# Optimization experiments

Hardware: AMD Instinct MI355X
Metric: run time of the kernel (lower is better)

## Reference

```python
import jax, jax.numpy as jnp
import numpy as np

N, L, S, E, H = 8, 4096, 4096, 256, 8
D = E // H
EPS = 1e-6


def setup_inputs() -> dict:
    key = jax.random.key(0)
    ks = jax.random.split(key, 12)
    sc = 1.0 / np.sqrt(E)
    return {
        "q": jax.random.normal(ks[0], (N, L, E), jnp.float32),
        "k": jax.random.normal(ks[1], (N, S, E), jnp.float32),
        "v": jax.random.normal(ks[2], (N, S, E), jnp.float32),
        "q_mask": jax.random.uniform(ks[3], (N, L)) > 0.2,
        "kv_mask": jax.random.uniform(ks[4], (N, S)) > 0.2,
        "Wq": jax.random.normal(ks[5], (E, E), jnp.float32) * sc,
        "bq": jax.random.normal(ks[6], (E,), jnp.float32) * sc,
        "Wk": jax.random.normal(ks[7], (E, E), jnp.float32) * sc,
        "bk": jax.random.normal(ks[8], (E,), jnp.float32) * sc,
        "Wv": jax.random.normal(ks[9], (E, E), jnp.float32) * sc,
        "bv": jax.random.normal(ks[10], (E,), jnp.float32) * sc,
        "Wm": jax.random.normal(ks[11], (E, E), jnp.float32) * sc,
    }


def reference(q, k, v, q_mask, kv_mask, Wq, bq, Wk, bk, Wv, bv, Wm):
    n, l, _ = q.shape
    s = k.shape[1]
    # QKV projections (torch Linear: x @ W.T + b), split into heads
    Q = (q @ Wq.T + bq).reshape(n, l, H, D)
    K = (k @ Wk.T + bk).reshape(n, s, H, D)
    V = (v @ Wv.T + bv).reshape(n, s, H, D)
    # elu feature map (elu(x) + 1)
    Qf = jax.nn.elu(Q) + 1.0
    Kf = jax.nn.elu(K) + 1.0
    qm = q_mask.astype(Qf.dtype)[:, :, None, None]
    km = kv_mask.astype(Kf.dtype)[:, :, None, None]
    Qf = Qf * qm
    Kf = Kf * km
    Vm = V * km / s  # values / v_length
    # KV aggregation: [n,h,d,v]
    KV = jnp.einsum('nshd,nshv->nhdv', Kf, Vm)
    # normalizer Z: [n,l,h]
    Z = 1.0 / (jnp.einsum('nlhd,nhd->nlh', Qf, Kf.sum(axis=1)) + EPS)
    out = jnp.einsum('nlhd,nhdv->nlhv', Qf, KV) * Z[..., None] * s
    # merge projection (no bias)
    return out.reshape(n, l, H * D) @ Wm.T
```

## Files before the change

### kernel.cpp

```cpp
#include <hip/hip_runtime.h>

#define EPSF 1e-6f

typedef __bf16 bf16;
typedef bf16 bf16x4 __attribute__((ext_vector_type(4)));
typedef bf16 bf16x8 __attribute__((ext_vector_type(8)));
typedef float f32x4 __attribute__((ext_vector_type(4)));


__global__ __launch_bounds__(256) void prep(
    const float* __restrict__ Wq, const float* __restrict__ Wk,
    const float* __restrict__ Wv, const float* __restrict__ Wm,
    bf16* __restrict__ Wb, float4* __restrict__ Z)
{
    const int b = blockIdx.x, t = threadIdx.x;
    if (b < 66) {
        const int i = b * 256 + t;
        if (i < 16896) Z[i] = float4{0.f, 0.f, 0.f, 0.f};
        return;
    }
    const int wi = b - 66;
    const int m  = wi >> 6;
    const float* S = (m == 0) ? Wq : (m == 1) ? Wk : (m == 2) ? Wv : Wm;
    const int idx = (wi & 63) * 1024 + t * 4;
    float4 v = *(const float4*)(S + idx);
    bf16x4 p = {(bf16)v.x, (bf16)v.y, (bf16)v.z, (bf16)v.w};
    *(bf16x4*)(Wb + (size_t)m * 65536 + idx) = p;
}

__global__ __launch_bounds__(256, 2) void kv_fused(
    const float* __restrict__ kin, const float* __restrict__ vin,
    const bf16* __restrict__ Wkb, const bf16* __restrict__ Wvb,
    const float* __restrict__ bk, const float* __restrict__ bv,
    const int* __restrict__ kv_mask,
    float* __restrict__ KV, float* __restrict__ Ksum)
{
    const int n = blockIdx.y, s0 = blockIdx.x * 32;
    const int t = threadIdx.x, lane = t & 63, w = t >> 6;
    const int ln15 = lane & 15, lg = lane >> 4;
    const int wn = w * 64;

    __shared__ bf16 Xs[32][40];
    __shared__ bf16 Ws[256][40];
    __shared__ bf16 KfT[256][40];
    __shared__ bf16 VmT[256][40];

    const int xr = t >> 3, xc = (t & 7) * 4;
    const int wr = t >> 2, wc = (t & 3) * 8;

    for (int g = 0; g < 2; ++g) {
        const float* X  = g ? vin : kin;
        const bf16*  Wg = g ? Wvb : Wkb;
        const float* bg = g ? bv : bk;
        f32x4 acc[2][4] = {};
        for (int k0 = 0; k0 < 256; k0 += 32) {
            float4 xv = *(const float4*)(X + ((size_t)(n * 4096 + s0 + xr)) * 256 + k0 + xc);
            bf16x4 xp = {(bf16)xv.x, (bf16)xv.y, (bf16)xv.z, (bf16)xv.w};
            *(bf16x4*)&Xs[xr][xc] = xp;
            #pragma unroll
            for (int i = 0; i < 4; ++i)
                *(bf16x8*)&Ws[wr + 64 * i][wc] =
                    *(const bf16x8*)(Wg + (size_t)(wr + 64 * i) * 256 + k0 + wc);
            __syncthreads();
            bf16x8 a[2], bfr[4];
            a[0] = *(const bf16x8*)&Xs[ln15][lg * 8];
            a[1] = *(const bf16x8*)&Xs[16 + ln15][lg * 8];
            #pragma unroll
            for (int ni = 0; ni < 4; ++ni)
                bfr[ni] = *(const bf16x8*)&Ws[wn + ni * 16 + ln15][lg * 8];
            #pragma unroll
            for (int mi = 0; mi < 2; ++mi)
                #pragma unroll
                for (int ni = 0; ni < 4; ++ni)
                    acc[mi][ni] = __builtin_amdgcn_mfma_f32_16x16x32_bf16(
                        a[mi], bfr[ni], acc[mi][ni], 0, 0, 0);
            __syncthreads();
        }
        bf16 (*T)[40] = g ? VmT : KfT;
        #pragma unroll
        for (int ni = 0; ni < 4; ++ni) {
            const int col = wn + ni * 16 + ln15;
            const float bias = bg[col];
            float red = 0.f;
            #pragma unroll
            for (int mi = 0; mi < 2; ++mi) {
                const int sb = mi * 16 + lg * 4;
                bf16x4 pk;
                #pragma unroll
                for (int r = 0; r < 4; ++r) {
                    float x = acc[mi][ni][r] + bias;
                    if (g == 0) x = (x > 0.f) ? (x + 1.f) : __expf(x);
                    x *= kv_mask[n * 4096 + s0 + sb + r] ? 1.f : 0.f;
                    red += x;
                    pk[r] = (bf16)x;
                }
                *(bf16x4*)&T[col][sb] = pk;
            }
            if (g == 0) {
                red += __shfl_xor(red, 16);
                red += __shfl_xor(red, 32);
                if (lane < 16) atomicAdd(Ksum + n * 256 + col, red);
            }
        }
        __syncthreads();
    }
    #pragma unroll
    for (int hh = 0; hh < 2; ++hh) {
        const int h = w * 2 + hh;
        bf16x8 a[2], bb[2];
        #pragma unroll
        for (int mi = 0; mi < 2; ++mi)
            a[mi] = *(const bf16x8*)&VmT[h * 32 + mi * 16 + ln15][lg * 8];
        #pragma unroll
        for (int ni = 0; ni < 2; ++ni)
            bb[ni] = *(const bf16x8*)&KfT[h * 32 + ni * 16 + ln15][lg * 8];
        float* base = KV + (size_t)(n * 8 + h) * 1024;
        #pragma unroll
        for (int mi = 0; mi < 2; ++mi)
            #pragma unroll
            for (int ni = 0; ni < 2; ++ni) {
                f32x4 c = {};
                c = __builtin_amdgcn_mfma_f32_16x16x32_bf16(a[mi], bb[ni], c, 0, 0, 0);
                const int d = ni * 16 + ln15;
                #pragma unroll
                for (int r = 0; r < 4; ++r) {
                    const int v = mi * 16 + lg * 4 + r;
                    atomicAdd(base + v * 32 + d, c[r]);
                }
            }
    }
}

__global__ __launch_bounds__(256, 2) void attn_fused(
    const float* __restrict__ qin, const bf16* __restrict__ Wqb,
    const float* __restrict__ bq, const int* __restrict__ q_mask,
    const bf16* __restrict__ Wmb,
    const float* __restrict__ KV, const float* __restrict__ Ksum,
    float* __restrict__ out)
{
    const int n = blockIdx.y, l0 = blockIdx.x * 32;
    const int t = threadIdx.x, lane = t & 63, w = t >> 6;
    const int ln15 = lane & 15, lg = lane >> 4;
    const int wn = w * 64;

    __shared__ bf16  Xs[32][40];
    __shared__ bf16  Ws[256][40];
    __shared__ bf16  Qs[32][264];
    __shared__ bf16  KVs[8][32][40];
    __shared__ float KSs[256];
    __shared__ float Dens[32][8];

    {
        const float* kvn = KV + (size_t)n * 8192;
        #pragma unroll
        for (int i = 0; i < 8; ++i) {
            const int idx = (t * 8 + i) * 4;
            float4 vv = *(const float4*)(kvn + idx);
            bf16x4 p = {(bf16)vv.x, (bf16)vv.y, (bf16)vv.z, (bf16)vv.w};
            const int h = idx >> 10, rem = idx & 1023;
            *(bf16x4*)&KVs[h][rem >> 5][rem & 31] = p;
        }
        KSs[t] = Ksum[n * 256 + t];
    }
    {
        const int xr = t >> 3, xc = (t & 7) * 4, wr = t >> 2, wc = (t & 3) * 8;
        f32x4 acc[2][4] = {};
        for (int k0 = 0; k0 < 256; k0 += 32) {
            float4 xv = *(const float4*)(qin + ((size_t)(n * 4096 + l0 + xr)) * 256 + k0 + xc);
            bf16x4 xp = {(bf16)xv.x, (bf16)xv.y, (bf16)xv.z, (bf16)xv.w};
            *(bf16x4*)&Xs[xr][xc] = xp;
            #pragma unroll
            for (int i = 0; i < 4; ++i)
                *(bf16x8*)&Ws[wr + 64 * i][wc] =
                    *(const bf16x8*)(Wqb + (size_t)(wr + 64 * i) * 256 + k0 + wc);
            __syncthreads();
            bf16x8 a[2], bfr[4];
            a[0] = *(const bf16x8*)&Xs[ln15][lg * 8];
            a[1] = *(const bf16x8*)&Xs[16 + ln15][lg * 8];
            #pragma unroll
            for (int ni = 0; ni < 4; ++ni)
                bfr[ni] = *(const bf16x8*)&Ws[wn + ni * 16 + ln15][lg * 8];
            #pragma unroll
            for (int mi = 0; mi < 2; ++mi)
                #pragma unroll
                for (int ni = 0; ni < 4; ++ni)
                    acc[mi][ni] = __builtin_amdgcn_mfma_f32_16x16x32_bf16(
                        a[mi], bfr[ni], acc[mi][ni], 0, 0, 0);
            __syncthreads();
        }
        #pragma unroll
        for (int ni = 0; ni < 4; ++ni) {
            const int col = wn + ni * 16 + ln15;
            const float bias = bq[col];
            #pragma unroll
            for (int mi = 0; mi < 2; ++mi)
                #pragma unroll
                for (int r = 0; r < 4; ++r) {
                    const int l = mi * 16 + lg * 4 + r;
                    float x = acc[mi][ni][r] + bias;
                    x = (x > 0.f) ? (x + 1.f) : __expf(x);
                    x *= q_mask[n * 4096 + l0 + l] ? 1.f : 0.f;
                    Qs[l][col] = (bf16)x;
                }
        }
    }
    __syncthreads();
    {
        const int l = t >> 3, h = t & 7;
        float s = 0.f;
        #pragma unroll
        for (int d = 0; d < 32; ++d)
            s += (float)Qs[l][h * 32 + d] * KSs[h * 32 + d];
        Dens[l][h] = s;
    }
    __syncthreads();
    #pragma unroll
    for (int hh = 0; hh < 2; ++hh) {
        const int h = w * 2 + hh;
        bf16x8 a[2], bb[2];
        #pragma unroll
        for (int mi = 0; mi < 2; ++mi)
            a[mi] = *(const bf16x8*)&KVs[h][mi * 16 + ln15][lg * 8];
        #pragma unroll
        for (int ni = 0; ni < 2; ++ni)
            bb[ni] = *(const bf16x8*)&Qs[ni * 16 + ln15][h * 32 + lg * 8];
        f32x4 c[2][2];
        #pragma unroll
        for (int mi = 0; mi < 2; ++mi)
            #pragma unroll
            for (int ni = 0; ni < 2; ++ni) {
                f32x4 z = {};
                c[mi][ni] = __builtin_amdgcn_mfma_f32_16x16x32_bf16(a[mi], bb[ni], z, 0, 0, 0);
            }
        #pragma unroll
        for (int ni = 0; ni < 2; ++ni) {
            const int l = ni * 16 + ln15;
            const float rcp = 1.f / (Dens[l][h] + EPSF);
            #pragma unroll
            for (int mi = 0; mi < 2; ++mi) {
                bf16x4 pk;
                #pragma unroll
                for (int r = 0; r < 4; ++r) pk[r] = (bf16)(c[mi][ni][r] * rcp);
                *(bf16x4*)&Qs[l][h * 32 + mi * 16 + lg * 4] = pk;
            }
        }
    }
    __syncthreads();
    {
        const int wr = t >> 2, wc = (t & 3) * 8;
        f32x4 acc[2][4] = {};
        for (int k0 = 0; k0 < 256; k0 += 32) {
            #pragma unroll
            for (int i = 0; i < 4; ++i)
                *(bf16x8*)&Ws[wr + 64 * i][wc] =
                    *(const bf16x8*)(Wmb + (size_t)(wr + 64 * i) * 256 + k0 + wc);
            __syncthreads();
            bf16x8 a[2], bfr[4];
            a[0] = *(const bf16x8*)&Qs[ln15][k0 + lg * 8];
            a[1] = *(const bf16x8*)&Qs[16 + ln15][k0 + lg * 8];
            #pragma unroll
            for (int ni = 0; ni < 4; ++ni)
                bfr[ni] = *(const bf16x8*)&Ws[wn + ni * 16 + ln15][lg * 8];
            #pragma unroll
            for (int mi = 0; mi < 2; ++mi)
                #pragma unroll
                for (int ni = 0; ni < 4; ++ni)
                    acc[mi][ni] = __builtin_amdgcn_mfma_f32_16x16x32_bf16(
                        a[mi], bfr[ni], acc[mi][ni], 0, 0, 0);
            __syncthreads();
        }
        #pragma unroll
        for (int ni = 0; ni < 4; ++ni) {
            const int col = wn + ni * 16 + ln15;
            #pragma unroll
            for (int mi = 0; mi < 2; ++mi)
                #pragma unroll
                for (int r = 0; r < 4; ++r) {
                    const int l = mi * 16 + lg * 4 + r;
                    out[((size_t)(n * 4096 + l0 + l)) * 256 + col] = acc[mi][ni][r];
                }
        }
    }
}

extern "C" void kernel_launch(void* const* d_in, const int* in_sizes, int n_in,
                              void* d_out, int out_size, void* d_ws, size_t ws_size,
                              hipStream_t stream) {
    const float* q      = (const float*)d_in[0];
    const float* k      = (const float*)d_in[1];
    const float* v      = (const float*)d_in[2];
    const int*   q_mask = (const int*)  d_in[3];
    const int*   kv_mask= (const int*)  d_in[4];
    const float* Wq     = (const float*)d_in[5];
    const float* bq     = (const float*)d_in[6];
    const float* Wk     = (const float*)d_in[7];
    const float* bk     = (const float*)d_in[8];
    const float* Wv     = (const float*)d_in[9];
    const float* bv     = (const float*)d_in[10];
    const float* Wm     = (const float*)d_in[11];

    char* ws = (char*)d_ws;
    float* KV   = (float*)ws;
    float* Ksum = (float*)(ws + 262144);
    bf16*  Wb   = (bf16*)(ws + 270336);
    bf16*  Wqb = Wb, *Wkb = Wb + 65536, *Wvb = Wb + 131072, *Wmb = Wb + 196608;

    const dim3 blk(256);
    prep<<<dim3(322), blk, 0, stream>>>(Wq, Wk, Wv, Wm, Wb, (float4*)ws);
    kv_fused<<<dim3(128, 8), blk, 0, stream>>>(k, v, Wkb, Wvb, bk, bv, kv_mask, KV, Ksum);
    attn_fused<<<dim3(128, 8), blk, 0, stream>>>(q, Wqb, bq, q_mask, Wmb, KV, Ksum, (float*)d_out);
}
```

Baseline: 233.2 us.

## Split KV pipeline into projection, chunked outer product and deterministic reduction

Replaces the fused KV kernel with three stages. The first projects K and V to transposed bf16 buffers in global memory. The second computes per-chunk KV partials and Ksum partials. The third reduces those partials, which removes the atomics and the workspace zeroing. The projection GEMMs now read operands straight from global memory without LDS staging or barriers, and use 64-row tiles instead of 32. This adds about 33 MB of extra global traffic for the intermediate and partial buffers, plus two more kernel launches.

```diff
diff --git a/kernel.cpp b/kernel.cpp
--- a/kernel.cpp
+++ b/kernel.cpp
@@ -8,205 +8,231 @@
 typedef float f32x4 __attribute__((ext_vector_type(4)));
 
 
-__global__ __launch_bounds__(256) void prep(
+__global__ __launch_bounds__(256) void wconv(
     const float* __restrict__ Wq, const float* __restrict__ Wk,
     const float* __restrict__ Wv, const float* __restrict__ Wm,
-    bf16* __restrict__ Wb, float4* __restrict__ Z)
+    bf16* __restrict__ Wb)
 {
     const int b = blockIdx.x, t = threadIdx.x;
-    if (b < 66) {
-        const int i = b * 256 + t;
-        if (i < 16896) Z[i] = float4{0.f, 0.f, 0.f, 0.f};
-        return;
-    }
-    const int wi = b - 66;
-    const int m  = wi >> 6;
+    const int m = b >> 6;
     const float* S = (m == 0) ? Wq : (m == 1) ? Wk : (m == 2) ? Wv : Wm;
-    const int idx = (wi & 63) * 1024 + t * 4;
+    const int idx = (b & 63) * 1024 + t * 4;
     float4 v = *(const float4*)(S + idx);
     bf16x4 p = {(bf16)v.x, (bf16)v.y, (bf16)v.z, (bf16)v.w};
     *(bf16x4*)(Wb + (size_t)m * 65536 + idx) = p;
 }
 
-__global__ __launch_bounds__(256, 2) void kv_fused(
-    const float* __restrict__ kin, const float* __restrict__ vin,
-    const bf16* __restrict__ Wkb, const bf16* __restrict__ Wvb,
+__global__ __launch_bounds__(256) void kv_proj(
+    const float* __restrict__ k, const float* __restrict__ v,
+    const bf16* __restrict__ Wb,
     const float* __restrict__ bk, const float* __restrict__ bv,
     const int* __restrict__ kv_mask,
-    float* __restrict__ KV, float* __restrict__ Ksum)
-{
-    const int n = blockIdx.y, s0 = blockIdx.x * 32;
+    bf16* __restrict__ KfT, bf16* __restrict__ VmT)
+{
+    const int z  = blockIdx.y;
+    const int m0 = blockIdx.x * 64;
     const int t = threadIdx.x, lane = t & 63, w = t >> 6;
     const int ln15 = lane & 15, lg = lane >> 4;
     const int wn = w * 64;
 
-    __shared__ bf16 Xs[32][40];
-    __shared__ bf16 Ws[256][40];
-    __shared__ bf16 KfT[256][40];
-    __shared__ bf16 VmT[256][40];
-
-    const int xr = t >> 3, xc = (t & 7) * 4;
-    const int wr = t >> 2, wc = (t & 3) * 8;
-
-    for (int g = 0; g < 2; ++g) {
-        const float* X  = g ? vin : kin;
-        const bf16*  Wg = g ? Wvb : Wkb;
-        const float* bg = g ? bv : bk;
-        f32x4 acc[2][4] = {};
-        for (int k0 = 0; k0 < 256; k0 += 32) {
-            float4 xv = *(const float4*)(X + ((size_t)(n * 4096 + s0 + xr)) * 256 + k0 + xc);
-            bf16x4 xp = {(bf16)xv.x, (bf16)xv.y, (bf16)xv.z, (bf16)xv.w};
-            *(bf16x4*)&Xs[xr][xc] = xp;
-            #pragma unroll
-            for (int i = 0; i < 4; ++i)
-                *(bf16x8*)&Ws[wr + 64 * i][wc] =
-                    *(const bf16x8*)(Wg + (size_t)(wr + 64 * i) * 256 + k0 + wc);
-            __syncthreads();
-            bf16x8 a[2], bfr[4];
-            a[0] = *(const bf16x8*)&Xs[ln15][lg * 8];
-            a[1] = *(const bf16x8*)&Xs[16 + ln15][lg * 8];
+    const float* X    = (z == 0) ? k : v;
+    const bf16*  W    = Wb + (size_t)(z + 1) * 65536;
+    const float* bias = (z == 0) ? bk : bv;
+
+    __shared__ bf16 T[64][264];
+
+    f32x4 acc[4][4] = {};
+    #pragma unroll 2
+    for (int k0 = 0; k0 < 256; k0 += 32) {
+        bf16x8 a[4], b[4];
+        #pragma unroll
+        for (int mi = 0; mi < 4; ++mi) {
+            const float* xp = X + (size_t)(m0 + mi * 16 + ln15) * 256 + k0 + lg * 8;
+            float4 x0 = *(const float4*)xp;
+            float4 x1 = *(const float4*)(xp + 4);
+            a[mi] = bf16x8{(bf16)x0.x, (bf16)x0.y, (bf16)x0.z, (bf16)x0.w,
+                           (bf16)x1.x, (bf16)x1.y, (bf16)x1.z, (bf16)x1.w};
+        }
+        #pragma unroll
+        for (int ni = 0; ni < 4; ++ni)
+            b[ni] = *(const bf16x8*)(W + (size_t)(wn + ni * 16 + ln15) * 256 + k0 + lg * 8);
+        #pragma unroll
+        for (int mi = 0; mi < 4; ++mi)
             #pragma unroll
             for (int ni = 0; ni < 4; ++ni)
-                bfr[ni] = *(const bf16x8*)&Ws[wn + ni * 16 + ln15][lg * 8];
-            #pragma unroll
-            for (int mi = 0; mi < 2; ++mi)
-                #pragma unroll
-                for (int ni = 0; ni < 4; ++ni)
-                    acc[mi][ni] = __builtin_amdgcn_mfma_f32_16x16x32_bf16(
-                        a[mi], bfr[ni], acc[mi][ni], 0, 0, 0);
-            __syncthreads();
-        }
-        bf16 (*T)[40] = g ? VmT : KfT;
-        #pragma unroll
-        for (int ni = 0; ni < 4; ++ni) {
-            const int col = wn + ni * 16 + ln15;
-            const float bias = bg[col];
-            float red = 0.f;
-            #pragma unroll
-            for (int mi = 0; mi < 2; ++mi) {
-                const int sb = mi * 16 + lg * 4;
-                bf16x4 pk;
-                #pragma unroll
-                for (int r = 0; r < 4; ++r) {
-                    float x = acc[mi][ni][r] + bias;
-                    if (g == 0) x = (x > 0.f) ? (x + 1.f) : __expf(x);
-                    x *= kv_mask[n * 4096 + s0 + sb + r] ? 1.f : 0.f;
-                    red += x;
-                    pk[r] = (bf16)x;
-                }
-                *(bf16x4*)&T[col][sb] = pk;
-            }
-            if (g == 0) {
-                red += __shfl_xor(red, 16);
-                red += __shfl_xor(red, 32);
-                if (lane < 16) atomicAdd(Ksum + n * 256 + col, red);
-            }
-        }
-        __syncthreads();
-    }
+                acc[mi][ni] = __builtin_amdgcn_mfma_f32_16x16x32_bf16(
+                    a[mi], b[ni], acc[mi][ni], 0, 0, 0);
+    }
+
+    float bb[4];
+    #pragma unroll
+    for (int ni = 0; ni < 4; ++ni) bb[ni] = bias[wn + ni * 16 + ln15];
+
+    #pragma unroll
+    for (int mi = 0; mi < 4; ++mi)
+        #pragma unroll
+        for (int r = 0; r < 4; ++r) {
+            const int row = mi * 16 + lg * 4 + r;
+            const float mv = kv_mask[m0 + row] ? 1.f : 0.f;
+            #pragma unroll
+            for (int ni = 0; ni < 4; ++ni) {
+                float x = acc[mi][ni][r] + bb[ni];
+                if (z == 0) x = (x > 0.f) ? (x + 1.f) : __expf(x);
+                T[row][wn + ni * 16 + ln15] = (bf16)(x * mv);
+            }
+        }
+    __syncthreads();
+
+    bf16* YT = (z == 0) ? KfT : VmT;
+    const int n = m0 >> 12, sl = m0 & 4095;
+    bf16* dst = YT + ((size_t)n * 256 + t) * 4096 + sl;
+    #pragma unroll
+    for (int j = 0; j < 8; ++j) {
+        bf16x8 vv;
+        #pragma unroll
+        for (int jj = 0; jj < 8; ++jj) vv[jj] = T[j * 8 + jj][t];
+        *(bf16x8*)(dst + j * 8) = vv;
+    }
+}
+
+__global__ __launch_bounds__(256) void kv_outer(
+    const bf16* __restrict__ KfT, const bf16* __restrict__ VmT,
+    float* __restrict__ part, float* __restrict__ part_ks)
+{
+    const int chunk = blockIdx.x, n = blockIdx.y;
+    const int s0 = chunk * 64;
+    const int t = threadIdx.x, lane = t & 63, w = t >> 6;
+    const int ln15 = lane & 15, lg = lane >> 4;
+
+    {
+        const bf16* kp = KfT + ((size_t)n * 256 + t) * 4096 + s0;
+        float s = 0.f;
+        #pragma unroll
+        for (int j = 0; j < 8; ++j) {
+            bf16x8 vv = *(const bf16x8*)(kp + j * 8);
+            #pragma unroll
+            for (int jj = 0; jj < 8; ++jj) s += (float)vv[jj];
+        }
+        part_ks[((size_t)n * 64 + chunk) * 256 + t] = s;
+    }
+
     #pragma unroll
     for (int hh = 0; hh < 2; ++hh) {
         const int h = w * 2 + hh;
-        bf16x8 a[2], bb[2];
+        f32x4 c2[2][2] = {};
+        #pragma unroll
+        for (int step = 0; step < 2; ++step) {
+            const int sb = s0 + step * 32 + lg * 8;
+            bf16x8 a[2], b[2];
+            #pragma unroll
+            for (int mi = 0; mi < 2; ++mi)
+                a[mi] = *(const bf16x8*)(KfT + ((size_t)n * 256 + h * 32 + mi * 16 + ln15) * 4096 + sb);
+            #pragma unroll
+            for (int nj = 0; nj < 2; ++nj)
+                b[nj] = *(const bf16x8*)(VmT + ((size_t)n * 256 + h * 32 + nj * 16 + ln15) * 4096 + sb);
+            #pragma unroll
+            for (int mi = 0; mi < 2; ++mi)
+                #pragma unroll
+                for (int nj = 0; nj < 2; ++nj)
+                    c2[mi][nj] = __builtin_amdgcn_mfma_f32_16x16x32_bf16(
+                        a[mi], b[nj], c2[mi][nj], 0, 0, 0);
+        }
+        float* pb = part + ((size_t)(n * 64 + chunk) * 8 + h) * 1024;
         #pragma unroll
         for (int mi = 0; mi < 2; ++mi)
-            a[mi] = *(const bf16x8*)&VmT[h * 32 + mi * 16 + ln15][lg * 8];
-        #pragma unroll
-        for (int ni = 0; ni < 2; ++ni)
-            bb[ni] = *(const bf16x8*)&KfT[h * 32 + ni * 16 + ln15][lg * 8];
-        float* base = KV + (size_t)(n * 8 + h) * 1024;
-        #pragma unroll
-        for (int mi = 0; mi < 2; ++mi)
-            #pragma unroll
-            for (int ni = 0; ni < 2; ++ni) {
-                f32x4 c = {};
-                c = __builtin_amdgcn_mfma_f32_16x16x32_bf16(a[mi], bb[ni], c, 0, 0, 0);
-                const int d = ni * 16 + ln15;
-                #pragma unroll
-                for (int r = 0; r < 4; ++r) {
-                    const int v = mi * 16 + lg * 4 + r;
-                    atomicAdd(base + v * 32 + d, c[r]);
-                }
-            }
-    }
-}
-
-__global__ __launch_bounds__(256, 2) void attn_fused(
-    const float* __restrict__ qin, const bf16* __restrict__ Wqb,
+            #pragma unroll
+            for (int nj = 0; nj < 2; ++nj)
+                *(f32x4*)(pb + (nj * 16 + ln15) * 32 + mi * 16 + lg * 4) = c2[mi][nj];
+    }
+}
+
+__global__ __launch_bounds__(256) void kv_reduce(
+    const float* __restrict__ part, const float* __restrict__ part_ks,
+    bf16* __restrict__ KVb, float* __restrict__ Ksum)
+{
+    const int nh = blockIdx.x, n = nh >> 3, h = nh & 7;
+    const int t = threadIdx.x;
+    f32x4 acc = {};
+    const float* p = part + ((size_t)n * 512 + h) * 1024 + t * 4;
+    for (int c = 0; c < 64; ++c)
+        acc += *(const f32x4*)(p + (size_t)c * 8192);
+    bf16x4 ob = {(bf16)acc[0], (bf16)acc[1], (bf16)acc[2], (bf16)acc[3]};
+    *(bf16x4*)(KVb + (size_t)nh * 1024 + t * 4) = ob;
+    if (t < 32) {
+        float s = 0.f;
+        const float* pk = part_ks + (size_t)n * 16384 + h * 32 + t;
+        for (int c = 0; c < 64; ++c) s += pk[c * 256];
+        Ksum[n * 256 + h * 32 + t] = s;
+    }
+}
+
+__global__ __launch_bounds__(256) void attn(
+    const float* __restrict__ qin, const bf16* __restrict__ Wb,
     const float* __restrict__ bq, const int* __restrict__ q_mask,
-    const bf16* __restrict__ Wmb,
-    const float* __restrict__ KV, const float* __restrict__ Ksum,
+    const bf16* __restrict__ KVb, const float* __restrict__ Ksum,
     float* __restrict__ out)
 {
-    const int n = blockIdx.y, l0 = blockIdx.x * 32;
+    const int n = blockIdx.y, l0 = blockIdx.x * 64;
+    const size_t row0 = (size_t)n * 4096 + l0;
     const int t = threadIdx.x, lane = t & 63, w = t >> 6;
     const int ln15 = lane & 15, lg = lane >> 4;
     const int wn = w * 64;
 
-    __shared__ bf16  Xs[32][40];
-    __shared__ bf16  Ws[256][40];
-    __shared__ bf16  Qs[32][264];
-    __shared__ bf16  KVs[8][32][40];
+    const bf16* Wq = Wb;
+    const bf16* Wm = Wb + 3 * 65536;
+
+    __shared__ bf16  Qs[64][264];
     __shared__ float KSs[256];
-    __shared__ float Dens[32][8];
+    __shared__ float Dens[64][9];
+
+    KSs[t] = Ksum[n * 256 + t];
 
     {
-        const float* kvn = KV + (size_t)n * 8192;
-        #pragma unroll
-        for (int i = 0; i < 8; ++i) {
-            const int idx = (t * 8 + i) * 4;
-            float4 vv = *(const float4*)(kvn + idx);
-            bf16x4 p = {(bf16)vv.x, (bf16)vv.y, (bf16)vv.z, (bf16)vv.w};
-            const int h = idx >> 10, rem = idx & 1023;
-            *(bf16x4*)&KVs[h][rem >> 5][rem & 31] = p;
-        }
-        KSs[t] = Ksum[n * 256 + t];
-    }
-    {
-        const int xr = t >> 3, xc = (t & 7) * 4, wr = t >> 2, wc = (t & 3) * 8;
-        f32x4 acc[2][4] = {};
+        f32x4 acc[4][4] = {};
+        #pragma unroll 2
         for (int k0 = 0; k0 < 256; k0 += 32) {
-            float4 xv = *(const float4*)(qin + ((size_t)(n * 4096 + l0 + xr)) * 256 + k0 + xc);
-            bf16x4 xp = {(bf16)xv.x, (bf16)xv.y, (bf16)xv.z, (bf16)xv.w};
-            *(bf16x4*)&Xs[xr][xc] = xp;
-            #pragma unroll
-            for (int i = 0; i < 4; ++i)
-                *(bf16x8*)&Ws[wr + 64 * i][wc] =
-                    *(const bf16x8*)(Wqb + (size_t)(wr + 64 * i) * 256 + k0 + wc);
-            __syncthreads();
-            bf16x8 a[2], bfr[4];
-            a[0] = *(const bf16x8*)&Xs[ln15][lg * 8];
-            a[1] = *(const bf16x8*)&Xs[16 + ln15][lg * 8];
+            bf16x8 a[4], b[4];
+            #pragma unroll
+            for (int mi = 0; mi < 4; ++mi) {
+                const float* xp = qin + (row0 + mi * 16 + ln15) * 256 + k0 + lg * 8;
+                float4 x0 = *(const float4*)xp;
+                float4 x1 = *(const float4*)(xp + 4);
+                a[mi] = bf16x8{(bf16)x0.x, (bf16)x0.y, (bf16)x0.z, (bf16)x0.w,
+                               (bf16)x1.x, (bf16)x1.y, (bf16)x1.z, (bf16)x1.w};
+            }
             #pragma unroll
             for (int ni = 0; ni < 4; ++ni)
-                bfr[ni] = *(const bf16x8*)&Ws[wn + ni * 16 + ln15][lg * 8];
-            #pragma unroll
-            for (int mi = 0; mi < 2; ++mi)
+                b[ni] = *(const bf16x8*)(Wq + (size_t)(wn + ni * 16 + ln15) * 256 + k0 + lg * 8);
+            #pragma unroll
+            for (int mi = 0; mi < 4; ++mi)
                 #pragma unroll
                 for (int ni = 0; ni < 4; ++ni)
                     acc[mi][ni] = __builtin_amdgcn_mfma_f32_16x16x32_bf16(
-                        a[mi], bfr[ni], acc[mi][ni], 0, 0, 0);
-            __syncthreads();
-        }
-        #pragma unroll
-        for (int ni = 0; ni < 4; ++ni) {
-            const int col = wn + ni * 16 + ln15;
-            const float bias = bq[col];
-            #pragma unroll
-            for (int mi = 0; mi < 2; ++mi)
-                #pragma unroll
-                for (int r = 0; r < 4; ++r) {
-                    const int l = mi * 16 + lg * 4 + r;
-                    float x = acc[mi][ni][r] + bias;
+                        a[mi], b[ni], acc[mi][ni], 0, 0, 0);
+        }
+        float bb[4];
+        #pragma unroll
+        for (int ni = 0; ni < 4; ++ni) bb[ni] = bq[wn + ni * 16 + ln15];
+        #pragma unroll
+        for (int mi = 0; mi < 4; ++mi)
+            #pragma unroll
+            for (int r = 0; r < 4; ++r) {
+                const int row = mi * 16 + lg * 4 + r;
+                const float mv = q_mask[row0 + row] ? 1.f : 0.f;
+                #pragma unroll
+                for (int ni = 0; ni < 4; ++ni) {
+                    float x = acc[mi][ni][r] + bb[ni];
                     x = (x > 0.f) ? (x + 1.f) : __expf(x);
-                    x *= q_mask[n * 4096 + l0 + l] ? 1.f : 0.f;
-                    Qs[l][col] = (bf16)x;
+                    Qs[row][wn + ni * 16 + ln15] = (bf16)(x * mv);
                 }
-        }
+            }
     }
     __syncthreads();
-    {
-        const int l = t >> 3, h = t & 7;
+
+    #pragma unroll
+    for (int i = 0; i < 2; ++i) {
+        const int idx = t + i * 256;
+        const int l = idx & 63, h = idx >> 6;
         float s = 0.f;
         #pragma unroll
         for (int d = 0; d < 32; ++d)
@@ -214,71 +240,67 @@
         Dens[l][h] = s;
     }
     __syncthreads();
+
     #pragma unroll
     for (int hh = 0; hh < 2; ++hh) {
         const int h = w * 2 + hh;
-        bf16x8 a[2], bb[2];
+        const bf16* kvh = KVb + (size_t)(n * 8 + h) * 1024;
+        bf16x8 a[2], b[4];
         #pragma unroll
         for (int mi = 0; mi < 2; ++mi)
-            a[mi] = *(const bf16x8*)&KVs[h][mi * 16 + ln15][lg * 8];
-        #pragma unroll
-        for (int ni = 0; ni < 2; ++ni)
-            bb[ni] = *(const bf16x8*)&Qs[ni * 16 + ln15][h * 32 + lg * 8];
-        f32x4 c[2][2];
+            a[mi] = *(const bf16x8*)(kvh + (mi * 16 + ln15) * 32 + lg * 8);
+        #pragma unroll
+        for (int nj = 0; nj < 4; ++nj)
+            b[nj] = *(const bf16x8*)&Qs[nj * 16 + ln15][h * 32 + lg * 8];
+        f32x4 c[2][4];
         #pragma unroll
         for (int mi = 0; mi < 2; ++mi)
             #pragma unroll
-            for (int ni = 0; ni < 2; ++ni) {
+            for (int nj = 0; nj < 4; ++nj) {
                 f32x4 z = {};
-                c[mi][ni] = __builtin_amdgcn_mfma_f32_16x16x32_bf16(a[mi], bb[ni], z, 0, 0, 0);
-            }
-        #pragma unroll
-        for (int ni = 0; ni < 2; ++ni) {
-            const int l = ni * 16 + ln15;
+                c[mi][nj] = __builtin_amdgcn_mfma_f32_16x16x32_bf16(a[mi], b[nj], z, 0, 0, 0);
+            }
+        #pragma unroll
+        for (int nj = 0; nj < 4; ++nj) {
+            const int l = nj * 16 + ln15;
             const float rcp = 1.f / (Dens[l][h] + EPSF);
             #pragma unroll
             for (int mi = 0; mi < 2; ++mi) {
                 bf16x4 pk;
                 #pragma unroll
-                for (int r = 0; r < 4; ++r) pk[r] = (bf16)(c[mi][ni][r] * rcp);
+                for (int r = 0; r < 4; ++r) pk[r] = (bf16)(c[mi][nj][r] * rcp);
                 *(bf16x4*)&Qs[l][h * 32 + mi * 16 + lg * 4] = pk;
             }
         }
     }
     __syncthreads();
+
     {
-        const int wr = t >> 2, wc = (t & 3) * 8;
-        f32x4 acc[2][4] = {};
+        f32x4 acc[4][4] = {};
+        #pragma unroll 2
         for (int k0 = 0; k0 < 256; k0 += 32) {
-            #pragma unroll
-            for (int i = 0; i < 4; ++i)
-                *(bf16x8*)&Ws[wr + 64 * i][wc] =
-                    *(const bf16x8*)(Wmb + (size_t)(wr + 64 * i) * 256 + k0 + wc);
-            __syncthreads();
-            bf16x8 a[2], bfr[4];
-            a[0] = *(const bf16x8*)&Qs[ln15][k0 + lg * 8];
-            a[1] = *(const bf16x8*)&Qs[16 + ln15][k0 + lg * 8];
+            bf16x8 a[4], b[4];
+            #pragma unroll
+            for (int mi = 0; mi < 4; ++mi)
+                a[mi] = *(const bf16x8*)&Qs[mi * 16 + ln15][k0 + lg * 8];
             #pragma unroll
             for (int ni = 0; ni < 4; ++ni)
-                bfr[ni] = *(const bf16x8*)&Ws[wn + ni * 16 + ln15][lg * 8];
-            #pragma unroll
-            for (int mi = 0; mi < 2; ++mi)
+                b[ni] = *(const bf16x8*)(Wm + (size_t)(wn + ni * 16 + ln15) * 256 + k0 + lg * 8);
+            #pragma unroll
+            for (int mi = 0; mi < 4; ++mi)
                 #pragma unroll
                 for (int ni = 0; ni < 4; ++ni)
                     acc[mi][ni] = __builtin_amdgcn_mfma_f32_16x16x32_bf16(
-                        a[mi], bfr[ni], acc[mi][ni], 0, 0, 0);
-            __syncthreads();
+                        a[mi], b[ni], acc[mi][ni], 0, 0, 0);
         }
         #pragma unroll
         for (int ni = 0; ni < 4; ++ni) {
             const int col = wn + ni * 16 + ln15;
             #pragma unroll
-            for (int mi = 0; mi < 2; ++mi)
-                #pragma unroll
-                for (int r = 0; r < 4; ++r) {
-                    const int l = mi * 16 + lg * 4 + r;
-                    out[((size_t)(n * 4096 + l0 + l)) * 256 + col] = acc[mi][ni][r];
-                }
+            for (int mi = 0; mi < 4; ++mi)
+                #pragma unroll
+                for (int r = 0; r < 4; ++r)
+                    out[(row0 + mi * 16 + lg * 4 + r) * 256 + col] = acc[mi][ni][r];
         }
     }
 }
@@ -300,13 +322,19 @@
     const float* Wm     = (const float*)d_in[11];
 
     char* ws = (char*)d_ws;
-    float* KV   = (float*)ws;
-    float* Ksum = (float*)(ws + 262144);
-    bf16*  Wb   = (bf16*)(ws + 270336);
-    bf16*  Wqb = Wb, *Wkb = Wb + 65536, *Wvb = Wb + 131072, *Wmb = Wb + 196608;
+    const size_t SZB = (size_t)8 * 4096 * 256 * sizeof(bf16);
+    bf16*  Wb      = (bf16*)ws;
+    bf16*  KfT     = (bf16*)(ws + 524288);
+    bf16*  VmT     = (bf16*)(ws + 524288 + SZB);
+    float* part    = (float*)(ws + 524288 + 2 * SZB);
+    float* part_ks = (float*)(ws + 524288 + 2 * SZB + 16777216);
+    bf16*  KVb     = (bf16*)(ws + 524288 + 2 * SZB + 16777216 + 524288);
+    float* Ksum    = (float*)(ws + 524288 + 2 * SZB + 16777216 + 524288 + 131072);
 
     const dim3 blk(256);
-    prep<<<dim3(322), blk, 0, stream>>>(Wq, Wk, Wv, Wm, Wb, (float4*)ws);
-    kv_fused<<<dim3(128, 8), blk, 0, stream>>>(k, v, Wkb, Wvb, bk, bv, kv_mask, KV, Ksum);
-    attn_fused<<<dim3(128, 8), blk, 0, stream>>>(q, Wqb, bq, q_mask, Wmb, KV, Ksum, (float*)d_out);
-}
+    wconv    <<<dim3(256),    blk, 0, stream>>>(Wq, Wk, Wv, Wm, Wb);
+    kv_proj  <<<dim3(512, 2), blk, 0, stream>>>(k, v, Wb, bk, bv, kv_mask, KfT, VmT);
+    kv_outer <<<dim3(64, 8),  blk, 0, stream>>>(KfT, VmT, part, part_ks);
+    kv_reduce<<<dim3(64),     blk, 0, stream>>>(part, part_ks, KVb, Ksum);
+    attn     <<<dim3(64, 8),  blk, 0, stream>>>(q, Wb, bq, q_mask, KVb, Ksum, (float*)d_out);
+}
```

New measurement: 251.2 us. 7.7% more time.
